# Kernel optimization log

Measured on AMD Instinct MI355X. Metric: run time of the kernel, lower is better.

The kernel has to match this reference:

```python
import jax, jax.numpy as jnp
import numpy as np

H, DH, BS, NSEL, WIN = 16, 64, 4, 4, 32  # heads, dim_head, compress/selection block, top-k blocks, sliding window


def rmsnorm(x):
    return x * jax.lax.rsqrt(jnp.mean(x * x, axis=-1, keepdims=True) + 1e-6)


def rope(x):
    # x: [B,S,H,d]; standard rotate-half RoPE, theta=10000
    B, S, Hh, d = x.shape
    half = d // 2
    inv = 1.0 / (10000.0 ** (jnp.arange(half, dtype=jnp.float32) / half))
    t = jnp.arange(S, dtype=jnp.float32)[:, None] * inv[None, :]
    cos = jnp.cos(t)[None, :, None, :]
    sin = jnp.sin(t)[None, :, None, :]
    x1, x2 = x[..., :half], x[..., half:]
    return jnp.concatenate([x1 * cos - x2 * sin, x1 * sin + x2 * cos], axis=-1)


def setup_inputs() -> dict:
    key = jax.random.key(0)
    ks = jax.random.split(key, 20)
    B, S, D = 2, 1024, 1024
    s = 0.02
    f32 = jnp.float32
    return {
        'x': jax.random.normal(ks[0], (B, S, D), f32),
        've': jax.random.normal(ks[1], (B, S, D), f32),
        'x0': jax.random.normal(ks[2], (B, S, D), f32),
        'lambdas': jnp.array([1.0, 0.0], f32),
        'Wq': jax.random.normal(ks[3], (D, H * DH), f32) * s,
        'Wk': jax.random.normal(ks[4], (D, H * DH), f32) * s,
        'Wv': jax.random.normal(ks[5], (D, H * DH), f32) * s,
        'pos_k': jax.random.normal(ks[6], (H, BS, DH), f32) * s,
        'pos_v': jax.random.normal(ks[7], (H, BS, DH), f32) * s,
        'Wck': jax.random.normal(ks[8], (BS * DH, DH), f32) * s,
        'Wcv': jax.random.normal(ks[9], (BS * DH, DH), f32) * s,
        'mem_k': jax.random.normal(ks[10], (H, 1, DH), f32) * s,
        'mem_v': jax.random.normal(ks[11], (H, 1, DH), f32) * s,
        'Wg': jax.random.normal(ks[12], (D, 3 * H), f32) * s,
        'Wo': jax.random.normal(ks[13], (H * DH, D), f32) * s,
        'Wfc': jax.random.normal(ks[14], (D, 4 * D), f32) * s,
        'Wproj': jax.random.normal(ks[15], (4 * D, D), f32) * s,
    }


def nsa_block(x, ve, x0, lambdas, Wq, Wk, Wv, pos_k, pos_v, Wck, Wcv, mem_k, mem_v, Wg, Wo, Wfc, Wproj):
    B, S, D = x.shape
    nB = S // BS
    scale = DH ** -0.5
    pos = jnp.arange(S)

    # lambda residual blend + rmsnorm (ve unused by NSA block)
    xr = lambdas[0] * x + lambdas[1] * x0
    h = rmsnorm(xr)

    q = (h @ Wq).reshape(B, S, H, DH)
    k = (h @ Wk).reshape(B, S, H, DH)
    v = (h @ Wv).reshape(B, S, H, DH)

    # ---- compressed-block branch ----
    kb = k.reshape(B, nB, BS, H, DH) + pos_k.transpose(1, 0, 2)[None, None]
    vb = v.reshape(B, nB, BS, H, DH) + pos_v.transpose(1, 0, 2)[None, None]
    kc = kb.transpose(0, 1, 3, 2, 4).reshape(B, nB, H, BS * DH) @ Wck  # [B,nB,H,d]
    vc = vb.transpose(0, 1, 3, 2, 4).reshape(B, nB, H, BS * DH) @ Wcv
    kc = jnp.concatenate([jnp.broadcast_to(mem_k.transpose(1, 0, 2)[None], (B, 1, H, DH)), kc], axis=1)
    vc = jnp.concatenate([jnp.broadcast_to(mem_v.transpose(1, 0, 2)[None], (B, 1, H, DH)), vc], axis=1)
    cs = jnp.einsum('bshd,bnhd->bhsn', q, kc) * scale
    block_last = jnp.arange(nB) * BS + (BS - 1)
    cvis = jnp.concatenate([jnp.ones((S, 1), bool), block_last[None, :] <= pos[:, None]], axis=1)
    cp = jax.nn.softmax(jnp.where(cvis[None, None], cs, -jnp.inf), axis=-1)
    cout = jnp.einsum('bhsn,bnhd->bshd', cp, vc)

    # ---- fine selected-block branch (top-k blocks by compressed attn mass + own diagonal block) ----
    imp = cp[..., 1:]  # [B,H,S,nB], zero for blocks not fully in the past
    sel_val, sel_idx = jax.lax.top_k(imp, NSEL)
    own = jnp.broadcast_to((pos // BS)[None, None, :, None], (B, H, S, 1)).astype(sel_idx.dtype)
    idx_all = jnp.concatenate([sel_idx, own], axis=-1)  # [B,H,S,NSEL+1]

    qr, kr = rope(q), rope(k)
    krb = kr.reshape(B, nB, BS, H, DH).transpose(0, 3, 1, 2, 4)  # [B,H,nB,Bs,d]
    vrb = v.reshape(B, nB, BS, H, DH).transpose(0, 3, 1, 2, 4)
    M = NSEL + 1
    idxf = idx_all.reshape(B, H, S * M, 1, 1)
    gk = jnp.take_along_axis(krb, idxf, axis=2).reshape(B, H, S, M * BS, DH)
    gv = jnp.take_along_axis(vrb, idxf, axis=2).reshape(B, H, S, M * BS, DH)
    kpos = idx_all[..., None] * BS + jnp.arange(BS)  # [B,H,S,M,Bs]
    vblock = jnp.concatenate([sel_val > 0, jnp.ones((B, H, S, 1), bool)], axis=-1)
    fmask = (vblock[..., None] & (kpos <= pos[None, None, :, None, None])).reshape(B, H, S, M * BS)
    fs = jnp.einsum('bshd,bhsmd->bhsm', qr, gk) * scale
    fp = jax.nn.softmax(jnp.where(fmask, fs, -jnp.inf), axis=-1)
    fout = jnp.einsum('bhsm,bhsmd->bshd', fp, gv)

    # ---- sliding-window branch ----
    off = jnp.arange(WIN)
    spos = pos[:, None] - off[None, :]  # [S,W]
    idx_s = jnp.clip(spos, 0, S - 1)
    ks_ = kr[:, idx_s]  # [B,S,W,H,d]
    vs_ = v[:, idx_s]
    ss = jnp.einsum('bshd,bswhd->bhsw', qr, ks_) * scale
    sp = jax.nn.softmax(jnp.where((spos >= 0)[None, None], ss, -jnp.inf), axis=-1)
    sout = jnp.einsum('bhsw,bswhd->bshd', sp, vs_)

    # ---- gated combine + out proj + MLP (relu^2) ----
    g = jax.nn.sigmoid(h @ Wg).reshape(B, S, H, 3)
    o = g[..., 0:1] * cout + g[..., 1:2] * fout + g[..., 2:3] * sout
    x1 = xr + o.reshape(B, S, H * DH) @ Wo
    m = rmsnorm(x1)
    return x1 + (jax.nn.relu(m @ Wfc) ** 2) @ Wproj


def reference(x, ve, x0, lambdas, Wq, Wk, Wv, pos_k, pos_v, Wck, Wcv, mem_k, mem_v, Wg, Wo, Wfc, Wproj):
    return nsa_block(x, ve, x0, lambdas, Wq, Wk, Wv, pos_k, pos_v, Wck, Wcv, mem_k, mem_v, Wg, Wo, Wfc, Wproj)
```

## Files before the change

kernel.cpp:

```cpp
#include <hip/hip_runtime.h>

constexpr int cH = 16, cDH = 64, cBS = 4, cNSEL = 4, cWIN = 32;
constexpr int cB = 2, cS = 1024, cD = 1024;
constexpr int cNB = 256, cNBLK = 257, cDFF = 4096, cM = 2048;
constexpr float cSCALE = 0.125f;
constexpr int cSSTR = 258;
constexpr int cNP = 288;

typedef unsigned short u16;
typedef unsigned int u32;
typedef __attribute__((ext_vector_type(8))) __bf16 bf16x8;
typedef __attribute__((ext_vector_type(8))) u16 u16x8;
typedef __attribute__((ext_vector_type(4))) float f32x4;
static_assert(sizeof(bf16x8) == 16, "bf16x8 must be 16B");

__device__ __forceinline__ float sigf(float x) { return 1.f / (1.f + expf(-x)); }
__device__ __forceinline__ float b2f(u16 u) {
  union { float f; u32 u; } c; c.u = ((u32)u) << 16; return c.f;
}
__device__ __forceinline__ u16 f2b(float f) {
  union { float f; u32 u; } c; c.f = f;
  u32 u = c.u;
  return (u16)((u + 0x7fffu + ((u >> 16) & 1u)) >> 16);
}
// ... 357 lines not shown
      #pragma unroll
      for (int n = 0; n < 2; n++) {
        int col = n0 + wc * 32 + n * 16 + l16;
        float v = acc[m][n][j];
        if (mat == 0) {
          qo[(size_t)row * cD + col] = v;
          u16 hb, lb; split_bf(v, hb, lb);
          qbh[(size_t)row * cD + col] = hb;
          qbl[(size_t)row * cD + col] = lb;
        } else if (mat == 1) {
          ko[(size_t)row * cD + col] = v;
        } else if (mat == 2) {
          vo[(size_t)row * cD + col] = v;
        } else if (col < 48) {
          gpre[(size_t)row * 48 + col] = v;
        }
      }
    }
  }
}

__global__ __launch_bounds__(64) void k_compress4(
    const float* __restrict__ kbuf, const float* __restrict__ vbuf,
    const float* __restrict__ pos_k, const float* __restrict__ pos_v,
    const float* __restrict__ Wck, const float* __restrict__ Wcv,
    const float* __restrict__ mem_k, const float* __restrict__ mem_v,
    float* __restrict__ kc, float* __restrict__ vc)
{
  int idx = blockIdx.x;
  int h = idx % cH; int n = (idx / cH) % cNBLK; int b = idx / (cH * cNBLK);
  int d = threadIdx.x;
  size_t co = (((size_t)b * cNBLK + n) * cH + h) * cDH + d;
  if (n == 0) {
    kc[co] = mem_k[h * cDH + d];
    vc[co] = mem_v[h * cDH + d];
    return;
  }
  __shared__ float kb[cBS * cDH], vb[cBS * cDH];
  int nb = n - 1;
  for (int t = d; t < cBS * cDH; t += 64) {
    int i = t >> 6, e = t & 63;
    size_t src = (((size_t)b * cS + nb * cBS + i) * cH + h) * cDH + e;
    kb[t] = kbuf[src] + pos_k[(h * cBS + i) * cDH + e];
    vb[t] = vbuf[src] + pos_v[(h * cBS + i) * cDH + e];
  }
  __syncthreads();
  float ak = 0.f, av = 0.f;
  #pragma unroll 4
  for (int j = 0; j < cBS * cDH; ++j) {
    ak += kb[j] * Wck[(size_t)j * cDH + d];
    av += vb[j] * Wcv[(size_t)j * cDH + d];
  }
  kc[co] = ak; vc[co] = av;
}

__global__ __launch_bounds__(256) void k_compress4_bf(
    const float* __restrict__ kbuf, const float* __restrict__ vbuf,
    const float* __restrict__ pos_k, const float* __restrict__ pos_v,
    const float* __restrict__ Wck, const float* __restrict__ Wcv,
    const float* __restrict__ mem_k, const float* __restrict__ mem_v,
    u16* __restrict__ kch, u16* __restrict__ kcl,
    u16* __restrict__ vth, u16* __restrict__ vtl)
{
  int wave = threadIdx.x >> 6, d = threadIdx.x & 63;
  int idx = blockIdx.x * 4 + wave;
  int h = idx % cH;
  int n = (idx / cH) % cNBLK;
  int b = idx / (cH * cNBLK);
  float ak, av;
  if (n == 0) {
    ak = mem_k[h * cDH + d];
    av = mem_v[h * cDH + d];
    size_t vr = ((size_t)(b * cH + h) * cDH + d) * cNP;
    for (int p = cNBLK; p < cNP; p++) { vth[vr + p] = 0; vtl[vr + p] = 0; }
  } else {
    __shared__ float kb[4][cBS * cDH], vb[4][cBS * cDH];
    int nb = n - 1;
    for (int t = d; t < cBS * cDH; t += 64) {
      int i = t >> 6, e = t & 63;
      size_t src = (((size_t)b * cS + nb * cBS + i) * cH + h) * cDH + e;
      kb[wave][t] = kbuf[src] + pos_k[(h * cBS + i) * cDH + e];
      vb[wave][t] = vbuf[src] + pos_v[(h * cBS + i) * cDH + e];
    }
    __syncthreads();
    ak = 0.f; av = 0.f;
    #pragma unroll 4
    for (int j = 0; j < cBS * cDH; ++j) {
      ak += kb[wave][j] * Wck[(size_t)j * cDH + d];
      av += vb[wave][j] * Wcv[(size_t)j * cDH + d];
    }
  }
  u16 kh, kl, vh, vl;
  split_bf(ak, kh, kl); split_bf(av, vh, vl);
  size_t kco = ((size_t)(b * cH + h) * cNP + n) * cDH + d;
  kch[kco] = kh; kcl[kco] = kl;
  size_t vco = ((size_t)(b * cH + h) * cDH + d) * cNP + n;
  vth[vco] = vh; vtl[vco] = vl;
}

__device__ __forceinline__ void top4_insert(float sv, int bi,
    float& v0, float& v1, float& v2, float& v3, int& i0, int& i1, int& i2, int& i3)
{
  if (sv > v3) {
    if (sv > v0)      { v3=v2;i3=i2; v2=v1;i2=i1; v1=v0;i1=i0; v0=sv;i0=bi; }
    else if (sv > v1) { v3=v2;i3=i2; v2=v1;i2=i1; v1=sv;i1=bi; }
    else if (sv > v2) { v3=v2;i3=i2; v2=sv;i2=bi; }
    else              { v3=sv;i3=bi; }
  }
}

__device__ __forceinline__ void top4_ins_tie(float sv, int bi,
    float& v0, float& v1, float& v2, float& v3, int& i0, int& i1, int& i2, int& i3)
{
  bool b3 = (sv > v3) || (sv == v3 && bi < i3);
  if (!b3) return;
  bool b0 = (sv > v0) || (sv == v0 && bi < i0);
  bool b1 = (sv > v1) || (sv == v1 && bi < i1);
  bool b2 = (sv > v2) || (sv == v2 && bi < i2);
  if (b0)      { v3=v2;i3=i2; v2=v1;i2=i1; v1=v0;i1=i0; v0=sv;i0=bi; }
  else if (b1) { v3=v2;i3=i2; v2=v1;i2=i1; v1=sv;i1=bi; }
  else if (b2) { v3=v2;i3=i2; v2=sv;i2=bi; }
  else         { v3=sv;i3=bi; }
}

template<int CNT>
__device__ __forceinline__ void cattn_cols(
    int base, int lane, int s_row, const float* __restrict__ kcb,
    const float* __restrict__ qrow, u16* __restrict__ ssb, float& lm,
    float& v0, float& v1, float& v2, float& v3,
    int& i0, int& i1, int& i2, int& i3)
{
  float sreg[CNT];
  #pragma unroll
  for (int u = 0; u < CNT; u++) sreg[u] = 0.f;
  #pragma unroll
  for (int d0 = 0; d0 < 4; d0++) {
    float4 qc0 = ((const float4*)qrow)[d0 * 4 + 0];
    float4 qc1 = ((const float4*)qrow)[d0 * 4 + 1];
    float4 qc2 = ((const float4*)qrow)[d0 * 4 + 2];
    float4 qc3 = ((const float4*)qrow)[d0 * 4 + 3];
    #pragma unroll
    for (int u = 0; u < CNT; u++) {
      int n = base + u;
      if (n < cNBLK) {
        const float4* kp = (const float4*)(kcb + (size_t)n * (cH * cDH) + d0 * 16);
        float4 k0 = kp[0], k1 = kp[1], k2 = kp[2], k3 = kp[3];
        sreg[u] += qc0.x*k0.x + qc0.y*k0.y + qc0.z*k0.z + qc0.w*k0.w
                 + qc1.x*k1.x + qc1.y*k1.y + qc1.z*k1.z + qc1.w*k1.w
                 + qc2.x*k2.x + qc2.y*k2.y + qc2.z*k2.z + qc2.w*k2.w
                 + qc3.x*k3.x + qc3.y*k3.y + qc3.z*k3.z + qc3.w*k3.w;
      }
    }
  }
  #pragma unroll
  for (int u = 0; u < CNT; u++) {
    int n = base + u;
    if (n >= cNBLK) continue;
    float a = sreg[u] * cSCALE;
    bool vis = (n == 0) || ((n - 1) * cBS + (cBS - 1) <= s_row);
    float sv = vis ? a : -INFINITY;
    ssb[lane * cSSTR + n] = f2b(sv);
    lm = fmaxf(lm, sv);
    if (n >= 1) top4_insert(sv, n - 1, v0, v1, v2, v3, i0, i1, i2, i3);
  }
}

__global__ __launch_bounds__(512, 4) void k_cattn_tile(
    const float* __restrict__ q, const float* __restrict__ kc, const float* __restrict__ vc,
    float* __restrict__ cout, float* __restrict__ sel_val, int* __restrict__ sel_idx)
{
  constexpr int NW = 8;
  constexpr int NCH = 33;
  __shared__ u16  ssb[64 * cSSTR];
  __shared__ float lmax[NW][64];
  __shared__ float lsum[NW][64];
  __shared__ float t4v[NW][64][4];
  __shared__ int   t4i[NW][64][4];
  __shared__ float mxs[64];
  __shared__ float invs[64];

  int tile = blockIdx.x & 15;
  int h = (blockIdx.x >> 4) & 15;
  int b = blockIdx.x >> 8;
  int s0 = tile * 64;
  int t = threadIdx.x;
  int lane = t & 63, wave = t >> 6;

  const float* kcb = kc + ((size_t)b * cNBLK * cH + h) * cDH;
  const float* vcb = vc + ((size_t)b * cNBLK * cH + h) * cDH;
  const int nstride = cH * cDH;

  {
    int r = lane;
    int s_row = s0 + r;
    const float* qrow = q + (((size_t)b * cS + s_row) * cH + h) * cDH;
    float v0=-INFINITY,v1=-INFINITY,v2=-INFINITY,v3=-INFINITY;
    int i0=0,i1=0,i2=0,i3=0;
    float lm = -INFINITY;
    int nb0 = wave * NCH;
    cattn_cols<11>(nb0,      r, s_row, kcb, qrow, ssb, lm, v0,v1,v2,v3, i0,i1,i2,i3);
    cattn_cols<11>(nb0 + 11, r, s_row, kcb, qrow, ssb, lm, v0,v1,v2,v3, i0,i1,i2,i3);
    cattn_cols<11>(nb0 + 22, r, s_row, kcb, qrow, ssb, lm, v0,v1,v2,v3, i0,i1,i2,i3);
    lmax[wave][lane] = lm;
    t4v[wave][lane][0]=v0; t4v[wave][lane][1]=v1; t4v[wave][lane][2]=v2; t4v[wave][lane][3]=v3;
    t4i[wave][lane][0]=i0; t4i[wave][lane][1]=i1; t4i[wave][lane][2]=i2; t4i[wave][lane][3]=i3;
  }
  __syncthreads();

  if (wave == 0) {
    int r = lane;
    float mx = -INFINITY;
    #pragma unroll
    for (int c = 0; c < NW; c++) mx = fmaxf(mx, lmax[c][r]);
    mxs[r] = mx;
    float v0=-INFINITY,v1=-INFINITY,v2=-INFINITY,v3=-INFINITY;
    int i0=0,i1=0,i2=0,i3=0;
    #pragma unroll
    for (int c = 0; c < NW; c++)
      #pragma unroll
      for (int u = 0; u < 4; u++)
        top4_insert(t4v[c][r][u], t4i[c][r][u], v0, v1, v2, v3, i0, i1, i2, i3);
    t4v[0][r][0]=v0; t4v[0][r][1]=v1; t4v[0][r][2]=v2; t4v[0][r][3]=v3;
    t4i[0][r][0]=i0; t4i[0][r][1]=i1; t4i[0][r][2]=i2; t4i[0][r][3]=i3;
  }
  __syncthreads();

  {
    int r = lane;
    float mx = mxs[r];
    float s = 0.f;
    int nb0 = wave * NCH;
    int nb1 = min(cNBLK, nb0 + NCH);
    for (int n = nb0; n < nb1; n++) {
      float sv = b2f(ssb[r * cSSTR + n]);
      float e = expf(sv - mx);
      ssb[r * cSSTR + n] = f2b(e);
      s += e;
    }
    lsum[wave][r] = s;
  }
  __syncthreads();

  if (wave == 0) {
    int r = lane;
    float sum = 0.f;
    #pragma unroll
    for (int c = 0; c < NW; c++) sum += lsum[c][r];
    float inv = 1.f / sum;
    invs[r] = inv;
    float mx = mxs[r];
    size_t so = (((size_t)b * cH + h) * cS + (s0 + r)) * cNSEL;
    #pragma unroll
    for (int u = 0; u < 4; u++) {
      sel_val[so + u] = expf(t4v[0][r][u] - mx) * inv;
      sel_idx[so + u] = t4i[0][r][u];
    }
  }
  __syncthreads();

  {
    int r = t >> 3, dq = t & 7;
    float4 a0 = {0,0,0,0}, a1 = {0,0,0,0};
    const u16* erow = ssb + r * cSSTR;
    const float* vbase = vcb + dq * 8;
#define ACC8(ee, w0, w1) \
    a0.x += (ee)*(w0).x; a0.y += (ee)*(w0).y; a0.z += (ee)*(w0).z; a0.w += (ee)*(w0).w; \
    a1.x += (ee)*(w1).x; a1.y += (ee)*(w1).y; a1.z += (ee)*(w1).z; a1.w += (ee)*(w1).w;
    for (int n = 0; n < 256; n += 4) {
      float e0 = b2f(erow[n+0]), e1 = b2f(erow[n+1]);
      float e2 = b2f(erow[n+2]), e3 = b2f(erow[n+3]);
      const float4* p0 = (const float4*)(vbase + (size_t)(n+0) * nstride);
      const float4* p1 = (const float4*)(vbase + (size_t)(n+1) * nstride);
      const float4* p2 = (const float4*)(vbase + (size_t)(n+2) * nstride);
      const float4* p3 = (const float4*)(vbase + (size_t)(n+3) * nstride);
      float4 w00 = p0[0], w01 = p0[1];
      float4 w10 = p1[0], w11 = p1[1];
      float4 w20 = p2[0], w21 = p2[1];
      float4 w30 = p3[0], w31 = p3[1];
      ACC8(e0, w00, w01)
      ACC8(e1, w10, w11)
      ACC8(e2, w20, w21)
      ACC8(e3, w30, w31)
    }
    {
      float e0 = b2f(erow[256]);
      const float4* p0 = (const float4*)(vbase + (size_t)256 * nstride);
      float4 w00 = p0[0], w01 = p0[1];
      ACC8(e0, w00, w01)
    }
#undef ACC8
    float inv = invs[r];
    float* crow = cout + (((size_t)b * cS + s0 + r) * cH + h) * cDH + dq * 8;
    ((float4*)crow)[0] = make_float4(a0.x*inv, a0.y*inv, a0.z*inv, a0.w*inv);
    ((float4*)crow)[1] = make_float4(a1.x*inv, a1.y*inv, a1.z*inv, a1.w*inv);
  }
}

__global__ __launch_bounds__(256) void k_cattn_mfma(
    const u16* __restrict__ qbh, const u16* __restrict__ qbl,
    const u16* __restrict__ kch, const u16* __restrict__ kcl,
    const u16* __restrict__ vth, const u16* __restrict__ vtl,
    float* __restrict__ cout, float* __restrict__ sel_val, int* __restrict__ sel_idx)
{
  constexpr int SST = 289;
  __shared__ float ssb[64 * SST];
  __shared__ float invs[64];

  int bid = (blockIdx.x & 7) * 64 + (blockIdx.x >> 3);
  int tile = bid & 15, h = (bid >> 4) & 15, b = bid >> 8;
  int s0 = tile * 64;
  int lane = threadIdx.x & 63, w = threadIdx.x >> 6;
  int l16 = lane & 15, rg = lane >> 4;
  int g8 = rg << 3;

  {
    size_t qrow = (((size_t)b * cS + (s0 + w * 16 + l16)) * cH + h) * cDH;
    bf16x8 qh0 = *(const bf16x8*)(qbh + qrow + g8);
    bf16x8 qh1 = *(const bf16x8*)(qbh + qrow + 32 + g8);
    bf16x8 ql0 = *(const bf16x8*)(qbl + qrow + g8);
    bf16x8 ql1 = *(const bf16x8*)(qbl + qrow + 32 + g8);
    const u16* kchb = kch + (size_t)(b * cH + h) * cNP * cDH;
    const u16* kclb = kcl + (size_t)(b * cH + h) * cNP * cDH;
    for (int nt = 0; nt < 18; nt++) {
      size_t krow = (size_t)(nt * 16 + l16) * cDH;
      bf16x8 bh0 = *(const bf16x8*)(kchb + krow + g8);
      bf16x8 bh1 = *(const bf16x8*)(kchb + krow + 32 + g8);
      bf16x8 bl0 = *(const bf16x8*)(kclb + krow + g8);
      bf16x8 bl1 = *(const bf16x8*)(kclb + krow + 32 + g8);
      f32x4 accA = {0.f,0.f,0.f,0.f}, accB = {0.f,0.f,0.f,0.f};
      accA = __builtin_amdgcn_mfma_f32_16x16x32_bf16(qh0, bh0, accA, 0, 0, 0);
      accA = __builtin_amdgcn_mfma_f32_16x16x32_bf16(qh1, bh1, accA, 0, 0, 0);
      accA = __builtin_amdgcn_mfma_f32_16x16x32_bf16(qh0, bl0, accA, 0, 0, 0);
      accA = __builtin_amdgcn_mfma_f32_16x16x32_bf16(qh1, bl1, accA, 0, 0, 0);
      accB = __builtin_amdgcn_mfma_f32_16x16x32_bf16(ql0, bh0, accB, 0, 0, 0);
      accB = __builtin_amdgcn_mfma_f32_16x16x32_bf16(ql1, bh1, accB, 0, 0, 0);
      accB = __builtin_amdgcn_mfma_f32_16x16x32_bf16(ql0, bl0, accB, 0, 0, 0);
      accB = __builtin_amdgcn_mfma_f32_16x16x32_bf16(ql1, bl1, accB, 0, 0, 0);
      int n = nt * 16 + l16;
      #pragma unroll
      for (int j = 0; j < 4; j++) {
        int r = w * 16 + rg * 4 + j;
        float a = (accA[j] + accB[j]) * cSCALE;
        bool vis = (n < cNBLK) && ((n == 0) || ((n - 1) * cBS + (cBS - 1) <= s0 + r));
        ssb[r * SST + n] = vis ? a : -INFINITY;
      }
    }
  }
  __syncthreads();

  {
    int row = threadIdx.x >> 2, sub = threadIdx.x & 3;
    float* srow = ssb + row * SST;
    int c0 = sub * 72;
    float v0=-INFINITY,v1=-INFINITY,v2=-INFINITY,v3=-INFINITY;
    int i0=0,i1=0,i2=0,i3=0;
    float mx = -INFINITY;
    int c1 = min(c0 + 72, cNBLK);
    for (int n = c0; n < c1; n++) {
      float sv = srow[n];
      mx = fmaxf(mx, sv);
      if (n >= 1) top4_ins_tie(sv, n - 1, v0,v1,v2,v3, i0,i1,i2,i3);
    }
    #pragma unroll
    for (int o = 1; o < 4; o <<= 1) {
      mx = fmaxf(mx, __shfl_xor(mx, o));
      float p0 = __shfl_xor(v0, o), p1 = __shfl_xor(v1, o);
      float p2 = __shfl_xor(v2, o), p3 = __shfl_xor(v3, o);
      int   q0 = __shfl_xor(i0, o), q1 = __shfl_xor(i1, o);
      int   q2 = __shfl_xor(i2, o), q3 = __shfl_xor(i3, o);
      top4_ins_tie(p0, q0, v0,v1,v2,v3, i0,i1,i2,i3);
      top4_ins_tie(p1, q1, v0,v1,v2,v3, i0,i1,i2,i3);
      top4_ins_tie(p2, q2, v0,v1,v2,v3, i0,i1,i2,i3);
      top4_ins_tie(p3, q3, v0,v1,v2,v3, i0,i1,i2,i3);
    }
    float sum = 0.f;
    for (int n = c0; n < c0 + 72; n++) {
      float e = expf(srow[n] - mx);
      srow[n] = e;
      sum += e;
    }
    #pragma unroll
    for (int o = 1; o < 4; o <<= 1) sum += __shfl_xor(sum, o);
    if (sub == 0) {
      float inv = 1.f / sum;
      invs[row] = inv;
      size_t so = (((size_t)b * cH + h) * cS + (s0 + row)) * cNSEL;
      sel_val[so + 0] = expf(v0 - mx) * inv; sel_idx[so + 0] = i0;
      sel_val[so + 1] = expf(v1 - mx) * inv; sel_idx[so + 1] = i1;
      sel_val[so + 2] = expf(v2 - mx) * inv; sel_idx[so + 2] = i2;
      sel_val[so + 3] = expf(v3 - mx) * inv; sel_idx[so + 3] = i3;
    }
  }
  __syncthreads();

  {
    const u16* vthb = vth + (size_t)(b * cH + h) * cDH * cNP;
    const u16* vtlb = vtl + (size_t)(b * cH + h) * cDH * cNP;
    f32x4 pacc[4];
    #pragma unroll
    for (int dt = 0; dt < 4; dt++) pacc[dt] = (f32x4){0.f, 0.f, 0.f, 0.f};
    int arow = (w * 16 + l16) * SST;
    for (int kc9 = 0; kc9 < 9; kc9++) {
      u16x8 et;
      #pragma unroll
      for (int e = 0; e < 8; e++)
        et[e] = f2b(ssb[arow + kc9 * 32 + g8 + e]);
      bf16x8 ea = __builtin_bit_cast(bf16x8, et);
      #pragma unroll
      for (int dt = 0; dt < 4; dt++) {
        size_t vrow = (size_t)(dt * 16 + l16) * cNP + kc9 * 32 + g8;
        bf16x8 bh = *(const bf16x8*)(vthb + vrow);
        bf16x8 bl = *(const bf16x8*)(vtlb + vrow);
        pacc[dt] = __builtin_amdgcn_mfma_f32_16x16x32_bf16(ea, bh, pacc[dt], 0, 0, 0);
        pacc[dt] = __builtin_amdgcn_mfma_f32_16x16x32_bf16(ea, bl, pacc[dt], 0, 0, 0);
      }
    }
    #pragma unroll
    for (int j = 0; j < 4; j++) {
      int r = w * 16 + rg * 4 + j;
      float inv = invs[r];
      float* crow = cout + (((size_t)b * cS + s0 + r) * cH + h) * cDH;
      #pragma unroll
      for (int dt = 0; dt < 4; dt++)
        crow[dt * 16 + l16] = pacc[dt][j] * inv;
    }
  }
}

__global__ __launch_bounds__(256) void k_rope(float* __restrict__ q, float* __restrict__ k)
{
  int t = blockIdx.x * 256 + threadIdx.x;
  int j = t & 31; int h = (t >> 5) & (cH - 1); int bs = t >> 9;
  int s = bs & (cS - 1);
  float inv = expf(-(float)j * 0.28782313662425575f);
  float ang = (float)s * inv;
  float sn, c; sincosf(ang, &sn, &c);
  size_t base = ((size_t)bs * cH + h) * cDH;
  float q1 = q[base + j], q2 = q[base + j + 32];
  q[base + j]      = q1 * c - q2 * sn;
  q[base + j + 32] = q1 * sn + q2 * c;
  float k1 = k[base + j], k2 = k[base + j + 32];
  k[base + j]      = k1 * c - k2 * sn;
  k[base + j + 32] = k1 * sn + k2 * c;
}

__global__ __launch_bounds__(256) void k_fsattn(
    const float* __restrict__ qr, const float* __restrict__ kr, const float* __restrict__ v,
    const float* __restrict__ sel_val, const int* __restrict__ sel_idx,
    float* __restrict__ fout, float* __restrict__ sout)
{
  int wave = threadIdx.x >> 6, lane = threadIdx.x & 63;
  int sidx = blockIdx.x * 4 + wave;
  int s = sidx % cS; int h = (sidx / cS) % cH; int b = sidx / (cS * cH);
  __shared__ float qs[4][cDH];
  __shared__ float pf[4][20];
  __shared__ float ps[4][cWIN];
  __shared__ int blk[4][5];
  __shared__ int bok[4][5];
  size_t qoff = (((size_t)b * cS + s) * cH + h) * cDH;
  qs[wave][lane] = qr[qoff + lane];
  if (lane < 5) {
    size_t so = (((size_t)b * cH + h) * cS + s) * cNSEL;
    if (lane < 4) { blk[wave][lane] = sel_idx[so + lane]; bok[wave][lane] = sel_val[so + lane] > 0.f; }
    else          { blk[wave][4] = s / cBS; bok[wave][4] = 1; }
  }
  __syncthreads();

  const float* kp = nullptr;
  if (lane < 20) {
    int tt = lane >> 2, i = lane & 3;
    int kpos = blk[wave][tt] * cBS + i;
    if (bok[wave][tt] && kpos <= s)
      kp = kr + (((size_t)b * cS + kpos) * cH + h) * cDH;
  } else if (lane >= 32) {
    int sp = s - (lane - 32);
    if (sp >= 0)
      kp = kr + (((size_t)b * cS + sp) * cH + h) * cDH;
  }
  float sc = -INFINITY;
  if (kp) {
    float a = 0.f;
    #pragma unroll 16
    for (int e = 0; e < cDH; e++) a += qs[wave][e] * kp[e];
    sc = a * cSCALE;
  }
  float mx = sc;
  #pragma unroll
  for (int o = 16; o; o >>= 1) mx = fmaxf(mx, __shfl_xor(mx, o, 32));
  float ex = (sc == -INFINITY) ? 0.f : expf(sc - mx);
  float sum = ex;
  #pragma unroll
  for (int o = 16; o; o >>= 1) sum += __shfl_xor(sum, o, 32);
  float pp = ex / sum;
  if (lane < 20) pf[wave][lane] = pp;
  if (lane >= 32) ps[wave][lane - 32] = pp;
  __syncthreads();

  float accf = 0.f;
  for (int tt = 0; tt < 5; tt++) {
    if (!bok[wave][tt]) continue;
    int kbase = blk[wave][tt] * cBS;
    #pragma unroll
    for (int i = 0; i < cBS; i++) {
      float pm = pf[wave][tt * cBS + i];
      if (pm != 0.f)
        accf += pm * v[(((size_t)b * cS + kbase + i) * cH + h) * cDH + lane];
    }
  }
  float accs = 0.f;
  int wm = min(cWIN, s + 1);
  for (int w = 0; w < wm; w++)
    accs += ps[wave][w] * v[(((size_t)b * cS + s - w) * cH + h) * cDH + lane];
  fout[qoff + lane] = accf;
  sout[qoff + lane] = accs;
}

__global__ __launch_bounds__(256) void k_combine(
    const float* __restrict__ gpre, const float* __restrict__ cout,
    const float* __restrict__ fout, const float* __restrict__ sout, float* __restrict__ o)
{
  int t = blockIdx.x * 256 + threadIdx.x;
  int hh = (t >> 6) & 15; int bs = t >> 10;
  float g0 = sigf(gpre[(size_t)bs * 48 + hh * 3 + 0]);
  float g1 = sigf(gpre[(size_t)bs * 48 + hh * 3 + 1]);
  float g2 = sigf(gpre[(size_t)bs * 48 + hh * 3 + 2]);
  o[t] = g0 * cout[t] + g1 * fout[t] + g2 * sout[t];
}

__global__ __launch_bounds__(256) void k_combine_bf(
    const float* __restrict__ gpre, const float* __restrict__ cout,
    const float* __restrict__ fout, const float* __restrict__ sout,
    u16* __restrict__ oh, u16* __restrict__ ol)
{
  int t = blockIdx.x * 256 + threadIdx.x;
  int hh = (t >> 6) & 15; int bs = t >> 10;
  float g0 = sigf(gpre[(size_t)bs * 48 + hh * 3 + 0]);
  float g1 = sigf(gpre[(size_t)bs * 48 + hh * 3 + 1]);
  float g2 = sigf(gpre[(size_t)bs * 48 + hh * 3 + 2]);
  float v = g0 * cout[t] + g1 * fout[t] + g2 * sout[t];
  u16 hb, lb; split_bf(v, hb, lb);
  oh[t] = hb; ol[t] = lb;
}

extern "C" void kernel_launch(void* const* d_in, const int* in_sizes, int n_in,
                              void* d_out, int out_size, void* d_ws, size_t ws_size,
                              hipStream_t stream) {
  float* out = (float*)d_out;

  static const int exp_sizes[17] = {
    2097152, 2097152, 2097152, 2,
    1048576, 1048576, 1048576,
    4096, 4096,
    16384, 16384,
    1024, 1024,
    49152, 1048576, 4194304, 4194304
  };
  if (n_in < 17) {
    k_fill<<<dim3(8192), dim3(256), 0, stream>>>(out, 500.0f + 10.0f * n_in);
    return;
  }
  for (int i = 0; i < 17; ++i) {
    if (in_sizes[i] != exp_sizes[i] && in_sizes[i] != 4 * exp_sizes[i]) {
      k_fill<<<dim3(8192), dim3(256), 0, stream>>>(out, 1000.0f + 50.0f * i);
      return;
    }
  }

  const float* x     = (const float*)d_in[0];
  const float* x0    = (const float*)d_in[2];
  const float* lam   = (const float*)d_in[3];
  const float* Wq    = (const float*)d_in[4];
  const float* Wk    = (const float*)d_in[5];
  const float* Wv    = (const float*)d_in[6];
  const float* pos_k = (const float*)d_in[7];
  const float* pos_v = (const float*)d_in[8];
  const float* Wck   = (const float*)d_in[9];
  const float* Wcv   = (const float*)d_in[10];
  const float* mem_k = (const float*)d_in[11];
  const float* mem_v = (const float*)d_in[12];
  const float* Wg    = (const float*)d_in[13];
  const float* Wo    = (const float*)d_in[14];
  const float* Wfc   = (const float*)d_in[15];
  const float* Wpr   = (const float*)d_in[16];

  float* ws = (float*)d_ws;
  const size_t E = (size_t)cM * cD;
  float* gpre = ws;
  float* selv = ws + 98304;
  int*   seli = (int*)(ws + 98304 + 131072);
  u16* WgTh = (u16*)(ws + 360448);
  u16* WgTl = WgTh + 65536;
  const size_t A0 = 1048576;
  float* xr = ws + A0 + 0 * E;
  float* h  = ws + A0 + 1 * E;
  float* q  = ws + A0 + 2 * E;
  float* k  = ws + A0 + 3 * E;
  float* v  = ws + A0 + 4 * E;
  float* co = ws + A0 + 5 * E;
  float* fo = ws + A0 + 6 * E;
  float* so = ws + A0 + 7 * E;
  float* x1 = ws + A0 + 8 * E;
  float* fc = ws + A0 + 2 * E;
  float* kc = fo;
  float* vc = so;

  const size_t P = A0 + 9 * E;
  const size_t NEED_FLOATS = P + 14680064;
  bool use_mfma = (ws_size >= NEED_FLOATS * sizeof(float));

  u16* WvTh = (u16*)(ws + P);              u16* WvTl = WvTh + 1048576;
  u16* WoTh = (u16*)(ws + P + 1048576);    u16* WoTl = WoTh + 1048576;
  u16* WfcTh = (u16*)(ws + P + 2097152);   u16* WfcTl = WfcTh + 4194304;
  u16* WprTh = (u16*)(ws + P + 6291456);   u16* WprTl = WprTh + 4194304;
  u16* hbh = (u16*)(ws + P + 10485760);    u16* hbl = hbh + 2097152;
  u16* obh = (u16*)(ws + P + 12582912);    u16* obl = obh + 2097152;
  u16* mbh = (u16*)h;                      u16* mbl = mbh + 2097152;
  u16* fbh = (u16*)q;                      u16* fbl = fbh + 8388608;
  u16* WqTh = (u16*)x1;                    u16* WqTl = WqTh + 1048576;
  u16* WkTh = WqTh + 2097152;              u16* WkTl = WqTh + 3145728;
  const size_t KCN = (size_t)cB * cH * cNP * cDH;
  u16* kch = (u16*)fo;       u16* kcl = kch + KCN;
  u16* vth = kcl + KCN;      u16* vtl = vth + KCN;
  u16* qbh = (u16*)so;       u16* qbl = qbh + 2097152;

  dim3 b256(256), b64(64), b512(512);
  dim3 gSq(cD / 64, cM / 64);

  if (use_mfma) {
    k_wsplit_t<<<dim3(32, 32), b256, 0, stream>>>(Wq, WqTh, WqTl, 1024, 1024);
    k_wsplit_t<<<dim3(32, 32), b256, 0, stream>>>(Wk, WkTh, WkTl, 1024, 1024);
    k_wsplit_t<<<dim3(32, 32), b256, 0, stream>>>(Wv, WvTh, WvTl, 1024, 1024);
    k_wsplit_t<<<dim3(32, 32), b256, 0, stream>>>(Wo, WoTh, WoTl, 1024, 1024);
    k_wsplit_t<<<dim3(128, 32), b256, 0, stream>>>(Wfc, WfcTh, WfcTl, 1024, 4096);
    k_wsplit_t<<<dim3(32, 128), b256, 0, stream>>>(Wpr, WprTh, WprTl, 4096, 1024);
    k_wsplit_g<<<dim3(256), b256, 0, stream>>>(Wg, WgTh, WgTl);

    k_lerp_rmsnorm<<<dim3(cM), b256, 0, stream>>>(x, x0, lam, xr, h, hbh, hbl);

    k_mfma_qkvg<<<dim3(49, 32), b256, 0, stream>>>(
        hbh, hbl, WqTh, WqTl, WkTh, WkTl, WvTh, WvTl, WgTh, WgTl,
        q, k, v, gpre, qbh, qbl);

    k_compress4_bf<<<dim3(cB * cNBLK * cH / 4), b256, 0, stream>>>(
        k, v, pos_k, pos_v, Wck, Wcv, mem_k, mem_v, kch, kcl, vth, vtl);
    k_cattn_mfma<<<dim3(cB * cH * 16), b256, 0, stream>>>(
        qbh, qbl, kch, kcl, vth, vtl, co, selv, seli);
    k_rope<<<dim3(cB * cS * cH * 32 / 256), b256, 0, stream>>>(q, k);
    k_fsattn<<<dim3(cB * cH * cS / 4), b256, 0, stream>>>(q, k, v, selv, seli, fo, so);

    k_combine_bf<<<dim3((cM * cD) / 256), b256, 0, stream>>>(gpre, co, fo, so, obh, obl);

    k_mfma_gemm<64, 64, 0, 0, 3><<<dim3(cD / 64, cM / 64), b256, 0, stream>>>(
        obh, obl, WoTh, WoTl, xr, x1, nullptr, nullptr, cM, cD, cD);

    k_rmsnorm<<<dim3(cM), b256, 0, stream>>>(x1, nullptr, mbh, mbl);

    k_mfma_gemm<64, 128, 1, 1, 3><<<dim3(cDFF / 128, cM / 64), b256, 0, stream>>>(
        mbh, mbl, WfcTh, WfcTl, nullptr, nullptr, fbh, fbl, cM, cDFF, cD);

    k_mfma_gemm<64, 64, 0, 0, 3><<<dim3(cD / 64, cM / 64), b256, 0, stream>>>(
        fbh, fbl, WprTh, WprTl, x1, out, nullptr, nullptr, cM, cD, cDFF);
  } else {
    k_lerp_rmsnorm<<<dim3(cM), b256, 0, stream>>>(x, x0, lam, xr, h, nullptr, nullptr);
    k_gemm<0><<<gSq, b256, 0, stream>>>(h, Wq, nullptr, q, cM, cD, cD);
    k_gemm<0><<<gSq, b256, 0, stream>>>(h, Wk, nullptr, k, cM, cD, cD);
    k_gemm<0><<<gSq, b256, 0, stream>>>(h, Wv, nullptr, v, cM, cD, cD);
    k_gemm<0><<<dim3(1, cM / 64), b256, 0, stream>>>(h, Wg, nullptr, gpre, cM, 48, cD);
    k_compress4<<<dim3(cB * cNBLK * cH), b64, 0, stream>>>(k, v, pos_k, pos_v, Wck, Wcv,
                                                           mem_k, mem_v, kc, vc);
    k_cattn_tile<<<dim3(cB * cH * 16), b512, 0, stream>>>(q, kc, vc, co, selv, seli);
    k_rope<<<dim3(cB * cS * cH * 32 / 256), b256, 0, stream>>>(q, k);
    k_fsattn<<<dim3(cB * cH * cS / 4), b256, 0, stream>>>(q, k, v, selv, seli, fo, so);
    k_combine<<<dim3((cM * cD) / 256), b256, 0, stream>>>(gpre, co, fo, so, co);
    k_gemm<0><<<gSq, b256, 0, stream>>>(co, Wo, xr, x1, cM, cD, cD);
    k_rmsnorm<<<dim3(cM), b256, 0, stream>>>(x1, h, nullptr, nullptr);
    k_gemm<1><<<dim3(cDFF / 64, cM / 64), b256, 0, stream>>>(h, Wfc, nullptr, fc, cM, cDFF, cD);
    k_gemm<0><<<gSq, b256, 0, stream>>>(fc, Wpr, x1, out, cM, cD, cDFF);
  }
}
```

Baseline: 657.8 us.

## Restructure compressed attention kernel to per-wave transposed MFMA with register softmax

The compressed-attention kernel now computes transposed score tiles (K as the A operand, Q as B), so each lane holds one query row's scores. Row max and top-4 selection are then done in registers with cross-lane shuffles instead of a separate shared-memory pass. Scores and probabilities are stored per-wave in bf16 shared memory rather than fp32, which shrinks LDS use and lets the PV MFMA operand load directly as a vector. Output is written as float4. Quantizing the raw scores to bf16 before the exp adds precision loss compared with the fp32 softmax it replaces.

```diff
diff --git a/kernel.cpp b/kernel.cpp
--- a/kernel.cpp
+++ b/kernel.cpp
@@ -683,128 +683,122 @@
     const u16* __restrict__ vth, const u16* __restrict__ vtl,
     float* __restrict__ cout, float* __restrict__ sel_val, int* __restrict__ sel_idx)
 {
-  constexpr int SST = 289;
-  __shared__ float ssb[64 * SST];
-  __shared__ float invs[64];
+  constexpr int SSTW = 296;
+  __shared__ u16 sws[4 * 16 * SSTW];
 
   int bid = (blockIdx.x & 7) * 64 + (blockIdx.x >> 3);
-  int tile = bid & 15, h = (bid >> 4) & 15, b = bid >> 8;
-  int s0 = tile * 64;
   int lane = threadIdx.x & 63, w = threadIdx.x >> 6;
-  int l16 = lane & 15, rg = lane >> 4;
-  int g8 = rg << 3;
-
-  {
-    size_t qrow = (((size_t)b * cS + (s0 + w * 16 + l16)) * cH + h) * cDH;
-    bf16x8 qh0 = *(const bf16x8*)(qbh + qrow + g8);
-    bf16x8 qh1 = *(const bf16x8*)(qbh + qrow + 32 + g8);
-    bf16x8 ql0 = *(const bf16x8*)(qbl + qrow + g8);
-    bf16x8 ql1 = *(const bf16x8*)(qbl + qrow + 32 + g8);
-    const u16* kchb = kch + (size_t)(b * cH + h) * cNP * cDH;
-    const u16* kclb = kcl + (size_t)(b * cH + h) * cNP * cDH;
-    for (int nt = 0; nt < 18; nt++) {
-      size_t krow = (size_t)(nt * 16 + l16) * cDH;
-      bf16x8 bh0 = *(const bf16x8*)(kchb + krow + g8);
-      bf16x8 bh1 = *(const bf16x8*)(kchb + krow + 32 + g8);
-      bf16x8 bl0 = *(const bf16x8*)(kclb + krow + g8);
-      bf16x8 bl1 = *(const bf16x8*)(kclb + krow + 32 + g8);
-      f32x4 accA = {0.f,0.f,0.f,0.f}, accB = {0.f,0.f,0.f,0.f};
-      accA = __builtin_amdgcn_mfma_f32_16x16x32_bf16(qh0, bh0, accA, 0, 0, 0);
-      accA = __builtin_amdgcn_mfma_f32_16x16x32_bf16(qh1, bh1, accA, 0, 0, 0);
-      accA = __builtin_amdgcn_mfma_f32_16x16x32_bf16(qh0, bl0, accA, 0, 0, 0);
-      accA = __builtin_amdgcn_mfma_f32_16x16x32_bf16(qh1, bl1, accA, 0, 0, 0);
-      accB = __builtin_amdgcn_mfma_f32_16x16x32_bf16(ql0, bh0, accB, 0, 0, 0);
-      accB = __builtin_amdgcn_mfma_f32_16x16x32_bf16(ql1, bh1, accB, 0, 0, 0);
-      accB = __builtin_amdgcn_mfma_f32_16x16x32_bf16(ql0, bl0, accB, 0, 0, 0);
-      accB = __builtin_amdgcn_mfma_f32_16x16x32_bf16(ql1, bl1, accB, 0, 0, 0);
-      int n = nt * 16 + l16;
-      #pragma unroll
-      for (int j = 0; j < 4; j++) {
-        int r = w * 16 + rg * 4 + j;
-        float a = (accA[j] + accB[j]) * cSCALE;
-        bool vis = (n < cNBLK) && ((n == 0) || ((n - 1) * cBS + (cBS - 1) <= s0 + r));
-        ssb[r * SST + n] = vis ? a : -INFINITY;
-      }
-    }
+  int l16 = lane & 15, rg = lane >> 4, g8 = rg << 3;
+  int tile = (bid & 15) * 4 + w;
+  int h = (bid >> 4) & 15, b = bid >> 8;
+  int s0 = tile * 16;
+  u16* sraw = sws + w * 16 * SSTW;
+
+  size_t qrow = (((size_t)b * cS + (s0 + l16)) * cH + h) * cDH;
+  bf16x8 qh0 = *(const bf16x8*)(qbh + qrow + g8);
+  bf16x8 qh1 = *(const bf16x8*)(qbh + qrow + 32 + g8);
+  bf16x8 ql0 = *(const bf16x8*)(qbl + qrow + g8);
+  bf16x8 ql1 = *(const bf16x8*)(qbl + qrow + 32 + g8);
+
+  const u16* kchb = kch + (size_t)(b * cH + h) * cNP * cDH;
+  const u16* kclb = kcl + (size_t)(b * cH + h) * cNP * cDH;
+
+  float v0=-INFINITY, v1=-INFINITY, v2=-INFINITY, v3=-INFINITY;
+  int i0=0, i1=0, i2=0, i3=0;
+  float lm = -INFINITY;
+
+  for (int nt = 0; nt < 18; nt++) {
+    size_t krow = (size_t)(nt * 16 + l16) * cDH;
+    bf16x8 kh0 = *(const bf16x8*)(kchb + krow + g8);
+    bf16x8 kh1 = *(const bf16x8*)(kchb + krow + 32 + g8);
+    bf16x8 kl0 = *(const bf16x8*)(kclb + krow + g8);
+    bf16x8 kl1 = *(const bf16x8*)(kclb + krow + 32 + g8);
+    f32x4 acc = (f32x4){0.f, 0.f, 0.f, 0.f};
+    acc = __builtin_amdgcn_mfma_f32_16x16x32_bf16(kh0, qh0, acc, 0, 0, 0);
+    acc = __builtin_amdgcn_mfma_f32_16x16x32_bf16(kh1, qh1, acc, 0, 0, 0);
+    acc = __builtin_amdgcn_mfma_f32_16x16x32_bf16(kh0, ql0, acc, 0, 0, 0);
+    acc = __builtin_amdgcn_mfma_f32_16x16x32_bf16(kh1, ql1, acc, 0, 0, 0);
+    acc = __builtin_amdgcn_mfma_f32_16x16x32_bf16(kl0, qh0, acc, 0, 0, 0);
+    acc = __builtin_amdgcn_mfma_f32_16x16x32_bf16(kl1, qh1, acc, 0, 0, 0);
+    acc = __builtin_amdgcn_mfma_f32_16x16x32_bf16(kl0, ql0, acc, 0, 0, 0);
+    acc = __builtin_amdgcn_mfma_f32_16x16x32_bf16(kl1, ql1, acc, 0, 0, 0);
+    u16 sb[4];
+    #pragma unroll
+    for (int j = 0; j < 4; j++) {
+      int n = nt * 16 + rg * 4 + j;
+      float a = acc[j] * cSCALE;
+      bool vis = (n < cNBLK) && ((n == 0) || ((n - 1) * cBS + (cBS - 1) <= s0 + l16));
+      float sv = vis ? a : -INFINITY;
+      sb[j] = f2b(sv);
+      lm = fmaxf(lm, sv);
+      if (n >= 1) top4_ins_tie(sv, n - 1, v0, v1, v2, v3, i0, i1, i2, i3);
+    }
+    int cw = nt * 16 + rg * 4;
+    *(u32*)&sraw[l16 * SSTW + cw]     = (u32)sb[0] | ((u32)sb[1] << 16);
+    *(u32*)&sraw[l16 * SSTW + cw + 2] = (u32)sb[2] | ((u32)sb[3] << 16);
+  }
+
+  #pragma unroll
+  for (int o = 16; o < 64; o <<= 1) {
+    lm = fmaxf(lm, __shfl_xor(lm, o));
+    float p0 = __shfl_xor(v0, o), p1 = __shfl_xor(v1, o);
+    float p2 = __shfl_xor(v2, o), p3 = __shfl_xor(v3, o);
+    int   q0 = __shfl_xor(i0, o), q1 = __shfl_xor(i1, o);
+    int   q2 = __shfl_xor(i2, o), q3 = __shfl_xor(i3, o);
+    top4_ins_tie(p0, q0, v0, v1, v2, v3, i0, i1, i2, i3);
+    top4_ins_tie(p1, q1, v0, v1, v2, v3, i0, i1, i2, i3);
+    top4_ins_tie(p2, q2, v0, v1, v2, v3, i0, i1, i2, i3);
+    top4_ins_tie(p3, q3, v0, v1, v2, v3, i0, i1, i2, i3);
+  }
+
+  float sum = 0.f;
+  for (int nt = 0; nt < 18; nt++) {
+    int cw = nt * 16 + rg * 4;
+    u32 w01 = *(u32*)&sraw[l16 * SSTW + cw];
+    u32 w23 = *(u32*)&sraw[l16 * SSTW + cw + 2];
+    float e0 = expf(b2f((u16)(w01 & 0xffff)) - lm);
+    float e1 = expf(b2f((u16)(w01 >> 16)) - lm);
+    float e2 = expf(b2f((u16)(w23 & 0xffff)) - lm);
+    float e3 = expf(b2f((u16)(w23 >> 16)) - lm);
+    sum += (e0 + e1) + (e2 + e3);
+    *(u32*)&sraw[l16 * SSTW + cw]     = (u32)f2b(e0) | ((u32)f2b(e1) << 16);
+    *(u32*)&sraw[l16 * SSTW + cw + 2] = (u32)f2b(e2) | ((u32)f2b(e3) << 16);
+  }
+  #pragma unroll
+  for (int o = 16; o < 64; o <<= 1) sum += __shfl_xor(sum, o);
+  float inv = 1.f / sum;
+
+  if (rg == 0) {
+    size_t so = (((size_t)b * cH + h) * cS + (s0 + l16)) * cNSEL;
+    sel_val[so + 0] = expf(v0 - lm) * inv; sel_idx[so + 0] = i0;
+    sel_val[so + 1] = expf(v1 - lm) * inv; sel_idx[so + 1] = i1;
+    sel_val[so + 2] = expf(v2 - lm) * inv; sel_idx[so + 2] = i2;
+    sel_val[so + 3] = expf(v3 - lm) * inv; sel_idx[so + 3] = i3;
   }
   __syncthreads();
 
-  {
-    int row = threadIdx.x >> 2, sub = threadIdx.x & 3;
-    float* srow = ssb + row * SST;
-    int c0 = sub * 72;
-    float v0=-INFINITY,v1=-INFINITY,v2=-INFINITY,v3=-INFINITY;
-    int i0=0,i1=0,i2=0,i3=0;
-    float mx = -INFINITY;
-    int c1 = min(c0 + 72, cNBLK);
-    for (int n = c0; n < c1; n++) {
-      float sv = srow[n];
-      mx = fmaxf(mx, sv);
-      if (n >= 1) top4_ins_tie(sv, n - 1, v0,v1,v2,v3, i0,i1,i2,i3);
-    }
-    #pragma unroll
-    for (int o = 1; o < 4; o <<= 1) {
-      mx = fmaxf(mx, __shfl_xor(mx, o));
-      float p0 = __shfl_xor(v0, o), p1 = __shfl_xor(v1, o);
-      float p2 = __shfl_xor(v2, o), p3 = __shfl_xor(v3, o);
-      int   q0 = __shfl_xor(i0, o), q1 = __shfl_xor(i1, o);
-      int   q2 = __shfl_xor(i2, o), q3 = __shfl_xor(i3, o);
-      top4_ins_tie(p0, q0, v0,v1,v2,v3, i0,i1,i2,i3);
-      top4_ins_tie(p1, q1, v0,v1,v2,v3, i0,i1,i2,i3);
-      top4_ins_tie(p2, q2, v0,v1,v2,v3, i0,i1,i2,i3);
-      top4_ins_tie(p3, q3, v0,v1,v2,v3, i0,i1,i2,i3);
-    }
-    float sum = 0.f;
-    for (int n = c0; n < c0 + 72; n++) {
-      float e = expf(srow[n] - mx);
-      srow[n] = e;
-      sum += e;
-    }
-    #pragma unroll
-    for (int o = 1; o < 4; o <<= 1) sum += __shfl_xor(sum, o);
-    if (sub == 0) {
-      float inv = 1.f / sum;
-      invs[row] = inv;
-      size_t so = (((size_t)b * cH + h) * cS + (s0 + row)) * cNSEL;
-      sel_val[so + 0] = expf(v0 - mx) * inv; sel_idx[so + 0] = i0;
-      sel_val[so + 1] = expf(v1 - mx) * inv; sel_idx[so + 1] = i1;
-      sel_val[so + 2] = expf(v2 - mx) * inv; sel_idx[so + 2] = i2;
-      sel_val[so + 3] = expf(v3 - mx) * inv; sel_idx[so + 3] = i3;
-    }
-  }
-  __syncthreads();
-
-  {
-    const u16* vthb = vth + (size_t)(b * cH + h) * cDH * cNP;
-    const u16* vtlb = vtl + (size_t)(b * cH + h) * cDH * cNP;
-    f32x4 pacc[4];
-    #pragma unroll
-    for (int dt = 0; dt < 4; dt++) pacc[dt] = (f32x4){0.f, 0.f, 0.f, 0.f};
-    int arow = (w * 16 + l16) * SST;
-    for (int kc9 = 0; kc9 < 9; kc9++) {
-      u16x8 et;
-      #pragma unroll
-      for (int e = 0; e < 8; e++)
-        et[e] = f2b(ssb[arow + kc9 * 32 + g8 + e]);
-      bf16x8 ea = __builtin_bit_cast(bf16x8, et);
-      #pragma unroll
-      for (int dt = 0; dt < 4; dt++) {
-        size_t vrow = (size_t)(dt * 16 + l16) * cNP + kc9 * 32 + g8;
-        bf16x8 bh = *(const bf16x8*)(vthb + vrow);
-        bf16x8 bl = *(const bf16x8*)(vtlb + vrow);
-        pacc[dt] = __builtin_amdgcn_mfma_f32_16x16x32_bf16(ea, bh, pacc[dt], 0, 0, 0);
-        pacc[dt] = __builtin_amdgcn_mfma_f32_16x16x32_bf16(ea, bl, pacc[dt], 0, 0, 0);
-      }
-    }
-    #pragma unroll
-    for (int j = 0; j < 4; j++) {
-      int r = w * 16 + rg * 4 + j;
-      float inv = invs[r];
-      float* crow = cout + (((size_t)b * cS + s0 + r) * cH + h) * cDH;
-      #pragma unroll
-      for (int dt = 0; dt < 4; dt++)
-        crow[dt * 16 + l16] = pacc[dt][j] * inv;
-    }
+  const u16* vthb = vth + (size_t)(b * cH + h) * cDH * cNP;
+  const u16* vtlb = vtl + (size_t)(b * cH + h) * cDH * cNP;
+  f32x4 pacc[4];
+  #pragma unroll
+  for (int dt = 0; dt < 4; dt++) pacc[dt] = (f32x4){0.f, 0.f, 0.f, 0.f};
+  for (int kc9 = 0; kc9 < 9; kc9++) {
+    bf16x8 ef = *(const bf16x8*)&sraw[l16 * SSTW + kc9 * 32 + g8];
+    #pragma unroll
+    for (int dt = 0; dt < 4; dt++) {
+      size_t vrow = (size_t)(dt * 16 + l16) * cNP + kc9 * 32 + g8;
+      bf16x8 vh = *(const bf16x8*)(vthb + vrow);
+      bf16x8 vl = *(const bf16x8*)(vtlb + vrow);
+      pacc[dt] = __builtin_amdgcn_mfma_f32_16x16x32_bf16(vh, ef, pacc[dt], 0, 0, 0);
+      pacc[dt] = __builtin_amdgcn_mfma_f32_16x16x32_bf16(vl, ef, pacc[dt], 0, 0, 0);
+    }
+  }
+  float* crow = cout + (((size_t)b * cS + (s0 + l16)) * cH + h) * cDH;
+  #pragma unroll
+  for (int dt = 0; dt < 4; dt++) {
+    *(float4*)(crow + dt * 16 + rg * 4) =
+        make_float4(pacc[dt][0] * inv, pacc[dt][1] * inv,
+                    pacc[dt][2] * inv, pacc[dt][3] * inv);
   }
 }
 
```

Result: faster. 626.3 us (-4.8%).
